# Kernel optimization log

Measured on AMD Instinct MI355X. Metric: run time of the kernel, lower is better.

Reference implementation:

```python
import jax, jax.numpy as jnp
import numpy as np

N_NODES = 100000
N_EDGES = 3200000
HID = 16
MP_ROUNDS = 3


def _mlp(w1, b1, w2, b2, x):
    # channels-first MLP applied per edge/node: x is [C_in, E]
    h = jax.nn.relu(w1 @ x + b1[:, None])
    return w2 @ h + b2[:, None]


def setup_inputs() -> dict:
    key = jax.random.key(0)
    ks = jax.random.split(key, 20)
    s = lambda k, shp: jax.random.normal(k, shp, dtype=jnp.float32) * 0.1
    inp = {
        "nodes": jax.random.normal(ks[0], (N_NODES,), dtype=jnp.float32),
        "edges_init": jax.random.normal(ks[1], (N_EDGES,), dtype=jnp.float32),
        "senders": jax.random.randint(ks[2], (N_EDGES,), 0, N_NODES, dtype=jnp.int32),
        "receivers": jax.random.randint(ks[3], (N_EDGES,), 0, N_NODES, dtype=jnp.int32),
        # EdgeEncoder: 1 -> HID -> HID
        "enc_w1": s(ks[4], (HID, 1)), "enc_b1": jnp.zeros((HID,), jnp.float32),
        "enc_w2": s(ks[5], (HID, HID)), "enc_b2": jnp.zeros((HID,), jnp.float32),
        # Node update MLP: (1 + 2*HID) -> HID -> 1  (shared across rounds)
        "node_w1": s(ks[6], (HID, 1 + 2 * HID)), "node_b1": jnp.zeros((HID,), jnp.float32),
        "node_w2": s(ks[7], (1, HID)), "node_b2": jnp.zeros((1,), jnp.float32),
        # Edge update MLP: (HID + 2) -> HID -> HID  (shared across rounds)
        "edge_w1": s(ks[8], (HID, HID + 2)), "edge_b1": jnp.zeros((HID,), jnp.float32),
        "edge_w2": s(ks[9], (HID, HID)), "edge_b2": jnp.zeros((HID,), jnp.float32),
        # EdgeDecoder: HID -> HID -> 1
        "dec_w1": s(ks[10], (HID, HID)), "dec_b1": jnp.zeros((HID,), jnp.float32),
        "dec_w2": s(ks[11], (1, HID)), "dec_b2": jnp.zeros((1,), jnp.float32),
        "alpha": jnp.float32(0.1),
    }
    return inp


def reference(nodes, edges_init, senders, receivers,
              enc_w1, enc_b1, enc_w2, enc_b2,
              node_w1, node_b1, node_w2, node_b2,
              edge_w1, edge_b1, edge_w2, edge_b2,
              dec_w1, dec_b1, dec_w2, dec_b2, alpha):
    n_nodes = nodes.shape[0]
    norm = jnp.abs(edges_init).max()
    e = edges_init / norm                      # [E]
    e = _mlp(enc_w1, enc_b1, enc_w2, enc_b2, e[None, :])   # [HID, E]
    for _ in range(MP_ROUNDS):                 # shared-weight MP blocks
        # gather/scatter: aggregate edge features to nodes
        agg_s = jax.ops.segment_sum(e.T, senders, num_segments=n_nodes).T     # [HID, N]
        agg_r = jax.ops.segment_sum(e.T, receivers, num_segments=n_nodes).T   # [HID, N]
        node_in = jnp.concatenate([nodes[None, :], agg_s, agg_r], axis=0)     # [1+2H, N]
        nodes = _mlp(node_w1, node_b1, node_w2, node_b2, node_in)[0]          # [N]
        edge_in = jnp.concatenate([e, nodes[senders][None, :], nodes[receivers][None, :]], axis=0)  # [H+2, E]
        e = _mlp(edge_w1, edge_b1, edge_w2, edge_b2, edge_in)                 # [HID, E]
    e = _mlp(dec_w1, dec_b1, dec_w2, dec_b2, e)[0]          # [E]
    low_tri_data = edges_init + alpha * (e * norm)          # L = L + alpha*GNN(L)
    return low_tri_data
```

## Files before the change

kernel.cpp:

```cpp
#include <hip/hip_runtime.h>
#include <hip/hip_bf16.h>

#define N_NODES 100000
#define N_EDGES 3200000
#define HID 16
#define NB 256
#define NPB 391
#define SCAP 15360
#define RCAP 15360
#define FDEPTH 32
#define LCAP1 8704
#define LCAP2 26624

static constexpr int BLK = 256;

__device__ __forceinline__ float frelu(float x) { return fmaxf(x, 0.f); }
__device__ __forceinline__ float bflo(unsigned int u) {
  return __uint_as_float(u << 16);
}
__device__ __forceinline__ float bfhi(unsigned int u) {
  return __uint_as_float(u & 0xFFFF0000u);
}

__device__ __forceinline__ int find_bucket(const int* __restrict__ bstart,
                                           int i) {
  int lo = 0, hi = NB;
#pragma unroll
  for (int s = 0; s < 8; ++s) {
    int mid = (lo + hi) >> 1;
    if (i >= bstart[mid]) lo = mid; else hi = mid;
  }
  return lo;
}

union E16 {
  float4 f4[2];
  __hip_bfloat16 h[16];
};

__global__ __launch_bounds__(256) void k_norm(const float* __restrict__ edges,
                                              unsigned int* __restrict__ normbits) {
  float m = 0.f;
  for (int i = blockIdx.x * blockDim.x + threadIdx.x; i < N_EDGES;
       i += gridDim.x * blockDim.x)
    m = fmaxf(m, fabsf(edges[i]));
#pragma unroll
  for (int off = 32; off > 0; off >>= 1)
    m = fmaxf(m, __shfl_down(m, off, 64));
  __shared__ float smax[BLK / 64];
  if ((threadIdx.x & 63) == 0) smax[threadIdx.x >> 6] = m;
  __syncthreads();
  if (threadIdx.x == 0) {
    float b = smax[0];
#pragma unroll
    for (int w = 1; w < BLK / 64; ++w) b = fmaxf(b, smax[w]);
    atomicMax(normbits, __float_as_uint(b));
  }
}

__global__ __launch_bounds__(1024) void k_split(
    const int* __restrict__ senders, const int* __restrict__ receivers,
    const float* __restrict__ edges, int* __restrict__ gcnt,
    unsigned int* __restrict__ pM, float* __restrict__ pV,
    unsigned int* __restrict__ pO) {
  __shared__ __align__(16) unsigned int fM[NB][FDEPTH];
  __shared__ __align__(16) unsigned int fV[NB][FDEPTH];
  __shared__ __align__(16) unsigned int fO[NB][FDEPTH];
  __shared__ int fcnt[NB];
  const int t = threadIdx.x;
  if (t < NB) fcnt[t] = 0;
  __syncthreads();
  const int e0 = blockIdx.x * (N_EDGES / 256);
  const int e1 = e0 + (N_EDGES / 256);
  for (int base = e0; base < e1; base += 1024) {
    const int i = base + t;
    if (i < e1) {
      int s = senders[i];
      unsigned int b = (unsigned int)s / NPB;
      unsigned int m = (((unsigned int)s - b * NPB) << 22) | (unsigned int)i;
      unsigned int v = __float_as_uint(edges[i]);
      unsigned int o = (unsigned int)receivers[i];
      int pos = atomicAdd(&fcnt[b], 1);
      if (pos < FDEPTH) {
        fM[b][pos] = m; fV[b][pos] = v; fO[b][pos] = o;
      } else {
        int gb = atomicAdd(&gcnt[b], 1);
        if (gb < SCAP) {
          pM[(size_t)b * SCAP + gb] = m;
          pV[(size_t)b * SCAP + gb] = __uint_as_float(v);
          pO[(size_t)b * SCAP + gb] = o;
        }
      }
    }
    __syncthreads();
    const bool last = (base + 1024 >= e1);
    if (t < NB) {
      int c = fcnt[t]; if (c > FDEPTH) c = FDEPTH;
      int nf = last ? c : (c & ~15);
      if (nf > 0) {
        int gb = atomicAdd(&gcnt[t], nf);
        size_t db = (size_t)t * SCAP + gb;
        if ((gb & 3) == 0 && gb + nf <= SCAP) {
          int k = 0;
          for (; k + 4 <= nf; k += 4) {
            *(uint4*)(pM + db + k) = *(const uint4*)(&fM[t][k]);
            *(uint4*)((unsigned int*)pV + db + k) = *(const uint4*)(&fV[t][k]);
            *(uint4*)(pO + db + k) = *(const uint4*)(&fO[t][k]);
          }
          for (; k < nf; ++k) {
            pM[db + k] = fM[t][k]; pV[db + k] = __uint_as_float(fV[t][k]);
            pO[db + k] = fO[t][k];
          }
        } else {
          for (int k = 0; k < nf; ++k)
            if (gb + k < SCAP) {
              pM[db + k] = fM[t][k]; pV[db + k] = __uint_as_float(fV[t][k]);
              pO[db + k] = fO[t][k];
            }
        }
        int res = c - nf;
        for (int k = 0; k < res; ++k) {
          fM[t][k] = fM[t][nf + k]; fV[t][k] = fV[t][nf + k];
          fO[t][k] = fO[t][nf + k];
        }
        fcnt[t] = res;
      } else fcnt[t] = c;
    }
    __syncthreads();
  }
}

__global__ __launch_bounds__(1024) void k_bsort1(
    const unsigned int* __restrict__ pM, const float* __restrict__ pV,
    const unsigned int* __restrict__ pO, const int* __restrict__ gcnt,
    unsigned int* __restrict__ srecv, unsigned int* __restrict__ sorig,
    unsigned short* __restrict__ svalbf, int* __restrict__ soff,
    int* __restrict__ bstart) {
  __shared__ unsigned int sM[LCAP1];
  __shared__ float sV[LCAP1];
  __shared__ unsigned int sO[LCAP1];
  __shared__ int hist[NPB], pref[NPB + 1], sc[NPB], cur[NPB];
  __shared__ int bb[NB];
  __shared__ int base_s;
  const int b = blockIdx.x, t = threadIdx.x, nt = blockDim.x;
  if (t < NB) { int c = gcnt[t]; bb[t] = c > SCAP ? SCAP : c; }
  for (int k = t; k < NPB; k += nt) hist[k] = 0;
  __syncthreads();
  if (t == 0) { int s = 0; for (int k = 0; k < b; ++k) s += bb[k]; base_s = s; }
  int nb = gcnt[b]; if (nb > SCAP) nb = SCAP;
  const unsigned int* PM = pM + (size_t)b * SCAP;
  const float* PV = pV + (size_t)b * SCAP;
  const unsigned int* PO = pO + (size_t)b * SCAP;
  for (int i = t; i < nb; i += nt) atomicAdd(&hist[PM[i] >> 22], 1);
  __syncthreads();
  if (t < NPB) sc[t] = hist[t];
  __syncthreads();
  for (int d = 1; d < NPB; d <<= 1) {
    int add = 0;
    if (t < NPB && t >= d) add = sc[t - d];
    __syncthreads();
    if (t < NPB && t >= d) sc[t] += add;
    __syncthreads();
  }
  if (t < NPB) pref[t] = sc[t] - hist[t];
  if (t == 0) pref[NPB] = sc[NPB - 1];
  __syncthreads();
  const int base = base_s;
  const int node0 = b * NPB;
  for (int k = t; k < NPB; k += nt) {
    int n = node0 + k;
    if (n < N_NODES) soff[n] = base + pref[k];
  }
  if (t == 0) bstart[b] = base;
  if (b == NB - 1 && t == 0) {
    soff[N_NODES] = base + nb;
    bstart[NB] = base + nb;
  }
  __syncthreads();
  int klo = 0;
  while (klo < NPB) {
    int base0 = pref[klo];
    int khi = klo;
    while (khi < NPB && pref[khi + 1] - base0 <= LCAP1) ++khi;
    if (khi == klo) khi = klo + 1;
    for (int k = klo + t; k < khi; k += nt) cur[k] = pref[k];
    __syncthreads();
    for (int i = t; i < nb; i += nt) {
      unsigned int m = PM[i];
      int key = (int)(m >> 22);
      if (key >= klo && key < khi) {
        int p = atomicAdd(&cur[key], 1) - base0;
        if (p < LCAP1) { sM[p] = m; sV[p] = PV[i]; sO[p] = PO[i]; }
      }
    }
    __syncthreads();
    int csz = pref[khi] - base0;
    for (int i = t; i < csz; i += nt) {
      int g = base + base0 + i;
      srecv[g] = sO[i]; sorig[g] = sM[i] & 0x3FFFFFu;
      __hip_bfloat16 hb = __float2bfloat16(sV[i]);
      svalbf[g] = *(unsigned short*)&hb;
    }
    __syncthreads();
    klo = khi;
  }
}

__global__ __launch_bounds__(256) void k_sfill(
    const int* __restrict__ soff, unsigned short* __restrict__ ssend16) {
  int wave = (blockIdx.x * blockDim.x + threadIdx.x) >> 6;
  int lane = threadIdx.x & 63, half = lane >> 5, l32 = lane & 31;
  int n = wave * 2 + half;
  unsigned short local = (unsigned short)(n - (n / NPB) * NPB);
  int s0 = soff[n], s1 = soff[n + 1];
  for (int k = s0 + l32; k < s1; k += 32) ssend16[k] = local;
}

__global__ __launch_bounds__(1024) void k_rsplit(
    const unsigned int* __restrict__ srecv, int* __restrict__ gcnt2,
    unsigned int* __restrict__ rpA) {
  __shared__ __align__(16) unsigned int fA[NB][FDEPTH];
  __shared__ int fcnt[NB];
  const int t = threadIdx.x;
  if (t < NB) fcnt[t] = 0;
  __syncthreads();
  const int e0 = blockIdx.x * (N_EDGES / 256);
  const int e1 = e0 + (N_EDGES / 256);
  for (int base = e0; base < e1; base += 1024) {
    const int i = base + t;
    if (i < e1) {
      unsigned int r = srecv[i];
      unsigned int b = r / NPB;
      unsigned int a = ((r - b * NPB) << 22) | (unsigned int)i;
      int pos = atomicAdd(&fcnt[b], 1);
      if (pos < FDEPTH) {
        fA[b][pos] = a;
      } else {
        int gb = atomicAdd(&gcnt2[b], 1);
        if (gb < RCAP) rpA[(size_t)b * RCAP + gb] = a;
      }
    }
    __syncthreads();
    const bool last = (base + 1024 >= e1);
    if (t < NB) {
      int c = fcnt[t]; if (c > FDEPTH) c = FDEPTH;
      int nf = last ? c : (c & ~15);
      if (nf > 0) {
        int gb = atomicAdd(&gcnt2[t], nf);
        size_t db = (size_t)t * RCAP + gb;
        if ((gb & 3) == 0 && gb + nf <= RCAP) {
          int k = 0;
          for (; k + 4 <= nf; k += 4)
            *(uint4*)(rpA + db + k) = *(const uint4*)(&fA[t][k]);
          for (; k < nf; ++k) rpA[db + k] = fA[t][k];
        } else {
          for (int k = 0; k < nf; ++k)
            if (gb + k < RCAP) rpA[db + k] = fA[t][k];
        }
        int res = c - nf;
        for (int k = 0; k < res; ++k) fA[t][k] = fA[t][nf + k];
        fcnt[t] = res;
      } else fcnt[t] = c;
    }
    __syncthreads();
  }
}

__global__ __launch_bounds__(1024) void k_rsort(
    const unsigned int* __restrict__ rpA, const int* __restrict__ gcnt2,
    unsigned int* __restrict__ rlist, int* __restrict__ roff) {
  __shared__ unsigned int sA[LCAP2];
  __shared__ int hist[NPB], pref[NPB + 1], sc[NPB], cur[NPB];
  __shared__ int bb[NB];
  __shared__ int base_s;
  const int b = blockIdx.x, t = threadIdx.x, nt = blockDim.x;
  if (t < NB) { int c = gcnt2[t]; bb[t] = c > RCAP ? RCAP : c; }
  for (int k = t; k < NPB; k += nt) hist[k] = 0;
  __syncthreads();
  if (t == 0) { int s = 0; for (int k = 0; k < b; ++k) s += bb[k]; base_s = s; }
  int nb = gcnt2[b]; if (nb > RCAP) nb = RCAP;
  const unsigned int* PA = rpA + (size_t)b * RCAP;
  for (int i = t; i < nb; i += nt) atomicAdd(&hist[PA[i] >> 22], 1);
  __syncthreads();
  if (t < NPB) sc[t] = hist[t];
  __syncthreads();
  for (int d = 1; d < NPB; d <<= 1) {
    int add = 0;
    if (t < NPB && t >= d) add = sc[t - d];
    __syncthreads();
    if (t < NPB && t >= d) sc[t] += add;
    __syncthreads();
  }
  if (t < NPB) pref[t] = sc[t] - hist[t];
  if (t == 0) pref[NPB] = sc[NPB - 1];
  __syncthreads();
  const int base = base_s;
  const int node0 = b * NPB;
  for (int k = t; k < NPB; k += nt) {
    int n = node0 + k;
    if (n < N_NODES) roff[n] = base + pref[k];
  }
  if (b == NB - 1 && t == 0) roff[N_NODES] = base + nb;
  __syncthreads();
  int klo = 0;
  while (klo < NPB) {
    int base0 = pref[klo];
    int khi = klo;
    while (khi < NPB && pref[khi + 1] - base0 <= LCAP2) ++khi;
    if (khi == klo) khi = klo + 1;
    for (int k = klo + t; k < khi; k += nt) cur[k] = pref[k];
    __syncthreads();
    for (int i = t; i < nb; i += nt) {
      unsigned int a = PA[i];
      int key = (int)(a >> 22);
      if (key >= klo && key < khi) {
        int p = atomicAdd(&cur[key], 1) - base0;
        if (p < LCAP2) sA[p] = a;
      }
    }
    __syncthreads();
    int csz = pref[khi] - base0;
    for (int i = t; i < csz; i += nt)
      rlist[base + base0 + i] = sA[i] & 0x3FFFFFu;
    __syncthreads();
    klo = khi;
  }
}

__global__ __launch_bounds__(256) void k_encode(
    const unsigned short* __restrict__ svalbf, const float* __restrict__ w1,
    const float* __restrict__ b1, const float* __restrict__ w2,
    const float* __restrict__ b2, const unsigned int* __restrict__ normbits,
    unsigned short* __restrict__ e) {
  int i = blockIdx.x * blockDim.x + threadIdx.x;
  float norm = __uint_as_float(*normbits);
  float x = bflo((unsigned int)svalbf[i]) / norm;
  float h[HID];
#pragma unroll
  for (int j = 0; j < HID; ++j) h[j] = frelu(fmaf(w1[j], x, b1[j]));
  E16 o;
#pragma unroll
  for (int j = 0; j < HID; ++j) {
    float acc = b2[j];
#pragma unroll
    for (int k = 0; k < HID; ++k) acc = fmaf(w2[j * HID + k], h[k], acc);
    o.h[j] = __float2bfloat16(acc);
  }
  float4* ep = (float4*)(e + (size_t)i * HID);
  ep[0] = o.f4[0];
  ep[1] = o.f4[1];
}

__global__ __launch_bounds__(256) void k_aggN(
    const unsigned short* __restrict__ e, const int* __restrict__ roff,
    const unsigned int* __restrict__ rlist, const int* __restrict__ soff,
    const float* __restrict__ nodesr, const float* __restrict__ nw1,
    const float* __restrict__ nb1_, const float* __restrict__ nw2,
    const float* __restrict__ nb2_, float* __restrict__ nodesw) {
  int wave = (blockIdx.x * blockDim.x + threadIdx.x) >> 6;
  int lane = threadIdx.x & 63, half = lane >> 5, l32 = lane & 31;
  int n = wave * 2 + half;
  int sub = l32 & 1, j16 = l32 >> 1;
  int r0 = roff[n], rdeg = roff[n + 1] - r0;
  float ar[8] = {0, 0, 0, 0, 0, 0, 0, 0};
  for (int q0 = 0; q0 < rdeg; q0 += 16) {
    int slot = q0 + j16;
    bool ok = slot < rdeg;
    int idx = r0 + (ok ? slot : 0);
    unsigned int si = rlist[idx];
    uint4 raw = *(const uint4*)(e + (size_t)si * HID + sub * 8);
    float v[8] = {bflo(raw.x), bfhi(raw.x), bflo(raw.y), bfhi(raw.y),
                  bflo(raw.z), bfhi(raw.z), bflo(raw.w), bfhi(raw.w)};
#pragma unroll
    for (int c = 0; c < 8; ++c) ar[c] += ok ? v[c] : 0.f;
  }
#pragma unroll
  for (int off = 16; off >= 2; off >>= 1)
#pragma unroll
    for (int c = 0; c < 8; ++c) ar[c] += __shfl_down(ar[c], off, 64);
  int s0 = soff[n], sdeg = soff[n + 1] - s0;
  float as[16];
#pragma unroll
  for (int c = 0; c < 16; ++c) as[c] = 0.f;
  for (int c0 = 0; c0 < sdeg; c0 += 32) {
    int k = c0 + l32;
    bool ok = k < sdeg;
    int idx = s0 + (ok ? k : 0);
    uint4 ra = *(const uint4*)(e + (size_t)idx * HID);
    uint4 rb = *(const uint4*)(e + (size_t)idx * HID + 8);
    float x[16] = {bflo(ra.x), bfhi(ra.x), bflo(ra.y), bfhi(ra.y),
                   bflo(ra.z), bfhi(ra.z), bflo(ra.w), bfhi(ra.w),
                   bflo(rb.x), bfhi(rb.x), bflo(rb.y), bfhi(rb.y),
                   bflo(rb.z), bfhi(rb.z), bflo(rb.w), bfhi(rb.w)};
#pragma unroll
    for (int c = 0; c < 16; ++c) as[c] += ok ? x[c] : 0.f;
  }
#pragma unroll
  for (int off = 16; off >= 1; off >>= 1)
#pragma unroll
    for (int c = 0; c < 16; ++c) as[c] += __shfl_down(as[c], off, 64);
  float aS[16], aR[16];
#pragma unroll
  for (int c = 0; c < 16; ++c) aS[c] = __shfl(as[c], half * 32, 64);
#pragma unroll
  for (int k = 0; k < 8; ++k) aR[k] = __shfl(ar[k], half * 32, 64);
#pragma unroll
  for (int k = 0; k < 8; ++k) aR[8 + k] = __shfl(ar[k], half * 32 + 1, 64);
  float nsv = nodesr[n];
  float pv = 0.f;
  if (l32 < 16) {
    int j = l32;
    float a1 = fmaf(nw1[j * 33], nsv, nb1_[j]);
#pragma unroll
    for (int k = 0; k < 16; ++k) a1 = fmaf(nw1[j * 33 + 1 + k], aS[k], a1);
#pragma unroll
    for (int k = 0; k < 16; ++k) a1 = fmaf(nw1[j * 33 + 17 + k], aR[k], a1);
    pv = nw2[j] * frelu(a1);
  }
#pragma unroll
  for (int off = 8; off >= 1; off >>= 1) pv += __shfl_down(pv, off, 64);
  if (l32 == 0) nodesw[n] = pv + nb2_[0];
}

__global__ __launch_bounds__(256, 2) void k_edgeE(
    unsigned short* __restrict__ e, const unsigned int* __restrict__ srecv,
    const unsigned short* __restrict__ ssend16, const int* __restrict__ bstart,
    const float* __restrict__ nodes, const float* __restrict__ w1,
    const float* __restrict__ b1, const float* __restrict__ w2,
    const float* __restrict__ b2) {
  int i = blockIdx.x * blockDim.x + threadIdx.x;
  int bk = find_bucket(bstart, i);
  int snd = bk * NPB + (int)ssend16[i];
  float ns = nodes[snd], nr = nodes[srecv[i]];
  uint4* ep = (uint4*)(e + (size_t)i * HID);
  uint4 ra = ep[0], rb = ep[1];
  unsigned int pk[8] = {ra.x, ra.y, ra.z, ra.w, rb.x, rb.y, rb.z, rb.w};
  float h[16];
#pragma unroll
  for (int j = 0; j < 16; ++j)
    h[j] = fmaf(w1[j * 18 + 16], ns, fmaf(w1[j * 18 + 17], nr, b1[j]));
#pragma unroll
  for (int kp = 0; kp < 8; ++kp) {
    float x0 = bflo(pk[kp]), x1 = bfhi(pk[kp]);
#pragma unroll
    for (int j = 0; j < 16; ++j)
      h[j] = fmaf(w1[j * 18 + 2 * kp + 1], x1,
                  fmaf(w1[j * 18 + 2 * kp], x0, h[j]));
  }
#pragma unroll
  for (int j = 0; j < 16; ++j) h[j] = frelu(h[j]);
  float y[16];
#pragma unroll
  for (int c = 0; c < 16; ++c) y[c] = b2[c];
#pragma unroll
  for (int j = 0; j < 16; ++j)
#pragma unroll
    for (int c = 0; c < 16; ++c) y[c] = fmaf(w2[c * HID + j], h[j], y[c]);
  E16 o;
#pragma unroll
  for (int c = 0; c < 16; ++c) o.h[c] = __float2bfloat16(y[c]);
  float4* fp = (float4*)ep;
  fp[0] = o.f4[0];
  fp[1] = o.f4[1];
}

__global__ __launch_bounds__(256, 2) void k_final(
    const unsigned short* __restrict__ e, const unsigned int* __restrict__ srecv,
    const unsigned short* __restrict__ ssend16, const int* __restrict__ bstart,
    const unsigned int* __restrict__ sorig, const float* __restrict__ nodes,
    const float* __restrict__ ew1, const float* __restrict__ eb1,
    const float* __restrict__ ew2, const float* __restrict__ eb2,
    const float* __restrict__ dw1, const float* __restrict__ db1,
    const float* __restrict__ dw2, const float* __restrict__ db2,
    const unsigned int* __restrict__ normbits, const float* __restrict__ alpha,
    float* __restrict__ out) {
  int i = blockIdx.x * blockDim.x + threadIdx.x;
  int bk = find_bucket(bstart, i);
  int snd = bk * NPB + (int)ssend16[i];
  float ns = nodes[snd], nr = nodes[srecv[i]];
  const uint4* ep = (const uint4*)(e + (size_t)i * HID);
  uint4 ra = ep[0], rb = ep[1];
  unsigned int pk[8] = {ra.x, ra.y, ra.z, ra.w, rb.x, rb.y, rb.z, rb.w};
  float h[16];
#pragma unroll
  for (int j = 0; j < 16; ++j)
    h[j] = fmaf(ew1[j * 18 + 16], ns, fmaf(ew1[j * 18 + 17], nr, eb1[j]));
#pragma unroll
  for (int kp = 0; kp < 8; ++kp) {
    float x0 = bflo(pk[kp]), x1 = bfhi(pk[kp]);
#pragma unroll
    for (int j = 0; j < 16; ++j)
      h[j] = fmaf(ew1[j * 18 + 2 * kp + 1], x1,
                  fmaf(ew1[j * 18 + 2 * kp], x0, h[j]));
  }
#pragma unroll
  for (int j = 0; j < 16; ++j) h[j] = frelu(h[j]);
  float y[16];
#pragma unroll
  for (int c = 0; c < 16; ++c) y[c] = eb2[c];
#pragma unroll
  for (int j = 0; j < 16; ++j)
#pragma unroll
    for (int c = 0; c < 16; ++c) y[c] = fmaf(ew2[c * HID + j], h[j], y[c]);
  float d = db2[0];
#pragma unroll
  for (int j = 0; j < 16; ++j) {
    float a1 = db1[j];
#pragma unroll
    for (int k = 0; k < 16; ++k) a1 = fmaf(dw1[j * HID + k], y[k], a1);
    d = fmaf(dw2[j], frelu(a1), d);
  }
  float alphaN = alpha[0] * __uint_as_float(*normbits);
  out[sorig[i]] = alphaN * d;
}

__global__ __launch_bounds__(256) void k_resid(const float* __restrict__ edges,
                                               float* __restrict__ out) {
  int i = blockIdx.x * blockDim.x + threadIdx.x;
  out[i] += edges[i];
}

extern "C" void kernel_launch(void* const* d_in, const int* in_sizes, int n_in,
                              void* d_out, int out_size, void* d_ws,
                              size_t ws_size, hipStream_t stream) {
  const float* nodes0 = (const float*)d_in[0];
  const float* edges0 = (const float*)d_in[1];
  const int* senders = (const int*)d_in[2];
  const int* receivers = (const int*)d_in[3];
  const float* enc_w1 = (const float*)d_in[4];
  const float* enc_b1 = (const float*)d_in[5];
  const float* enc_w2 = (const float*)d_in[6];
  const float* enc_b2 = (const float*)d_in[7];
  const float* node_w1 = (const float*)d_in[8];
  const float* node_b1 = (const float*)d_in[9];
  const float* node_w2 = (const float*)d_in[10];
  const float* node_b2 = (const float*)d_in[11];
  const float* edge_w1 = (const float*)d_in[12];
  const float* edge_b1 = (const float*)d_in[13];
  const float* edge_w2 = (const float*)d_in[14];
  const float* edge_b2 = (const float*)d_in[15];
  const float* dec_w1 = (const float*)d_in[16];
  const float* dec_b1 = (const float*)d_in[17];
  const float* dec_w2 = (const float*)d_in[18];
  const float* dec_b2 = (const float*)d_in[19];
  const float* alpha = (const float*)d_in[20];

  char* ws = (char*)d_ws;
  unsigned short* e = (unsigned short*)ws;
  char* p = ws + (size_t)N_EDGES * HID * 2;
  unsigned int* srecv = (unsigned int*)p;    p += (size_t)N_EDGES * 4;
  unsigned int* sorig = (unsigned int*)p;    p += (size_t)N_EDGES * 4;
  unsigned int* rlist = (unsigned int*)p;    p += (size_t)N_EDGES * 4;
  unsigned short* ssend16 = (unsigned short*)p; p += (size_t)N_EDGES * 2;
  unsigned short* svalbf = (unsigned short*)p;  p += (size_t)N_EDGES * 2;
  int* soff = (int*)p;                       p += (size_t)(N_NODES + 16) * 4;
  int* roff = (int*)p;                       p += (size_t)(N_NODES + 16) * 4;
  float* nbA = (float*)p;                    p += (size_t)N_NODES * 4;
  float* nbB = (float*)p;                    p += (size_t)N_NODES * 4;
  unsigned int* normbits = (unsigned int*)p; p += 64;
  int* gcnt = (int*)p;                       p += NB * 4;
  int* gcnt2 = (int*)p;                      p += NB * 4;
  int* bstart = (int*)p;                     p += (NB + 1) * 4;
  unsigned int* pM = (unsigned int*)ws;
  float* pV = (float*)(ws + (size_t)NB * SCAP * 4);
  unsigned int* pO = (unsigned int*)(ws + (size_t)NB * SCAP * 8);
  unsigned int* rpA = (unsigned int*)(ws + (size_t)NB * SCAP * 12);

  const int ngrid = 12500;
  const int egrid = N_EDGES / BLK;

  hipMemsetAsync(normbits, 0, 64 + 2 * NB * 4, stream);
  k_norm<<<512, BLK, 0, stream>>>(edges0, normbits);
  k_split<<<256, 1024, 0, stream>>>(senders, receivers, edges0, gcnt, pM, pV, pO);
  k_bsort1<<<NB, 1024, 0, stream>>>(pM, pV, pO, gcnt, srecv, sorig, svalbf,
                                    soff, bstart);
  k_sfill<<<ngrid, BLK, 0, stream>>>(soff, ssend16);
  k_rsplit<<<256, 1024, 0, stream>>>(srecv, gcnt2, rpA);
  k_rsort<<<NB, 1024, 0, stream>>>(rpA, gcnt2, rlist, roff);
  k_encode<<<egrid, BLK, 0, stream>>>(svalbf, enc_w1, enc_b1, enc_w2, enc_b2,
                                      normbits, e);
  k_aggN<<<ngrid, BLK, 0, stream>>>(e, roff, rlist, soff, nodes0, node_w1,
                                    node_b1, node_w2, node_b2, nbA);
  k_edgeE<<<egrid, BLK, 0, stream>>>(e, srecv, ssend16, bstart, nbA, edge_w1,
                                     edge_b1, edge_w2, edge_b2);
  k_aggN<<<ngrid, BLK, 0, stream>>>(e, roff, rlist, soff, nbA, node_w1,
                                    node_b1, node_w2, node_b2, nbB);
  k_edgeE<<<egrid, BLK, 0, stream>>>(e, srecv, ssend16, bstart, nbB, edge_w1,
                                     edge_b1, edge_w2, edge_b2);
  k_aggN<<<ngrid, BLK, 0, stream>>>(e, roff, rlist, soff, nbB, node_w1,
                                    node_b1, node_w2, node_b2, nbA);
  k_final<<<egrid, BLK, 0, stream>>>(e, srecv, ssend16, bstart, sorig, nbA,
                                     edge_w1, edge_b1, edge_w2, edge_b2,
                                     dec_w1, dec_b1, dec_w2, dec_b2, normbits,
                                     alpha, (float*)d_out);
  k_resid<<<egrid, BLK, 0, stream>>>(edges0, (float*)d_out);
}
```

Before: 918.2 us.

## Store full sender ids in bsort, drop sfill, multi-edge per thread edge kernels

The bucket sort now writes a 32-bit sender index per edge, which removes the k_sfill kernel and the per-edge binary search over bucket starts in the edge kernels. k_edgeE now processes 4 edges per thread and k_final 2, so weight loads are amortised across edges. k_aggN splits its gather loops into full unmasked iterations plus a masked tail. The trade-offs are extra bytes for the 32-bit sender array and higher register pressure in the multi-edge kernels.

```diff
diff --git a/kernel.cpp b/kernel.cpp
--- a/kernel.cpp
+++ b/kernel.cpp
@@ -21,16 +21,10 @@
 __device__ __forceinline__ float bfhi(unsigned int u) {
   return __uint_as_float(u & 0xFFFF0000u);
 }
-
-__device__ __forceinline__ int find_bucket(const int* __restrict__ bstart,
-                                           int i) {
-  int lo = 0, hi = NB;
-#pragma unroll
-  for (int s = 0; s < 8; ++s) {
-    int mid = (lo + hi) >> 1;
-    if (i >= bstart[mid]) lo = mid; else hi = mid;
-  }
-  return lo;
+__device__ __forceinline__ unsigned int packbf(float lo, float hi) {
+  __hip_bfloat16 hl = __float2bfloat16(lo), hh = __float2bfloat16(hi);
+  return ((unsigned int)(*(unsigned short*)&hh) << 16) |
+         (unsigned int)(*(unsigned short*)&hl);
 }
 
 union E16 {
@@ -134,8 +128,8 @@
     const unsigned int* __restrict__ pM, const float* __restrict__ pV,
     const unsigned int* __restrict__ pO, const int* __restrict__ gcnt,
     unsigned int* __restrict__ srecv, unsigned int* __restrict__ sorig,
-    unsigned short* __restrict__ svalbf, int* __restrict__ soff,
-    int* __restrict__ bstart) {
+    unsigned short* __restrict__ svalbf, unsigned int* __restrict__ ssend32,
+    int* __restrict__ soff) {
   __shared__ unsigned int sM[LCAP1];
   __shared__ float sV[LCAP1];
   __shared__ unsigned int sO[LCAP1];
@@ -171,11 +165,7 @@
     int n = node0 + k;
     if (n < N_NODES) soff[n] = base + pref[k];
   }
-  if (t == 0) bstart[b] = base;
-  if (b == NB - 1 && t == 0) {
-    soff[N_NODES] = base + nb;
-    bstart[NB] = base + nb;
-  }
+  if (b == NB - 1 && t == 0) soff[N_NODES] = base + nb;
   __syncthreads();
   int klo = 0;
   while (klo < NPB) {
@@ -197,23 +187,15 @@
     int csz = pref[khi] - base0;
     for (int i = t; i < csz; i += nt) {
       int g = base + base0 + i;
-      srecv[g] = sO[i]; sorig[g] = sM[i] & 0x3FFFFFu;
+      unsigned int m = sM[i];
+      srecv[g] = sO[i]; sorig[g] = m & 0x3FFFFFu;
+      ssend32[g] = (unsigned int)(node0 + (int)(m >> 22));
       __hip_bfloat16 hb = __float2bfloat16(sV[i]);
       svalbf[g] = *(unsigned short*)&hb;
     }
     __syncthreads();
     klo = khi;
   }
-}
-
-__global__ __launch_bounds__(256) void k_sfill(
-    const int* __restrict__ soff, unsigned short* __restrict__ ssend16) {
-  int wave = (blockIdx.x * blockDim.x + threadIdx.x) >> 6;
-  int lane = threadIdx.x & 63, half = lane >> 5, l32 = lane & 31;
-  int n = wave * 2 + half;
-  unsigned short local = (unsigned short)(n - (n / NPB) * NPB);
-  int s0 = soff[n], s1 = soff[n + 1];
-  for (int k = s0 + l32; k < s1; k += 32) ssend16[k] = local;
 }
 
 __global__ __launch_bounds__(1024) void k_rsplit(
@@ -363,16 +345,28 @@
   int sub = l32 & 1, j16 = l32 >> 1;
   int r0 = roff[n], rdeg = roff[n + 1] - r0;
   float ar[8] = {0, 0, 0, 0, 0, 0, 0, 0};
-  for (int q0 = 0; q0 < rdeg; q0 += 16) {
+  int fullA = rdeg & ~15;
+  int q0 = 0;
+  for (; q0 < fullA; q0 += 16) {
+    int idx = r0 + q0 + j16;
+    unsigned int si = rlist[idx];
+    uint4 raw = *(const uint4*)(e + (size_t)si * HID + sub * 8);
+    ar[0] += bflo(raw.x); ar[1] += bfhi(raw.x);
+    ar[2] += bflo(raw.y); ar[3] += bfhi(raw.y);
+    ar[4] += bflo(raw.z); ar[5] += bfhi(raw.z);
+    ar[6] += bflo(raw.w); ar[7] += bfhi(raw.w);
+  }
+  if (q0 < rdeg) {
     int slot = q0 + j16;
     bool ok = slot < rdeg;
     int idx = r0 + (ok ? slot : 0);
     unsigned int si = rlist[idx];
     uint4 raw = *(const uint4*)(e + (size_t)si * HID + sub * 8);
-    float v[8] = {bflo(raw.x), bfhi(raw.x), bflo(raw.y), bfhi(raw.y),
-                  bflo(raw.z), bfhi(raw.z), bflo(raw.w), bfhi(raw.w)};
-#pragma unroll
-    for (int c = 0; c < 8; ++c) ar[c] += ok ? v[c] : 0.f;
+    float okf = ok ? 1.f : 0.f;
+    ar[0] = fmaf(bflo(raw.x), okf, ar[0]); ar[1] = fmaf(bfhi(raw.x), okf, ar[1]);
+    ar[2] = fmaf(bflo(raw.y), okf, ar[2]); ar[3] = fmaf(bfhi(raw.y), okf, ar[3]);
+    ar[4] = fmaf(bflo(raw.z), okf, ar[4]); ar[5] = fmaf(bfhi(raw.z), okf, ar[5]);
+    ar[6] = fmaf(bflo(raw.w), okf, ar[6]); ar[7] = fmaf(bfhi(raw.w), okf, ar[7]);
   }
 #pragma unroll
   for (int off = 16; off >= 2; off >>= 1)
@@ -382,18 +376,36 @@
   float as[16];
 #pragma unroll
   for (int c = 0; c < 16; ++c) as[c] = 0.f;
-  for (int c0 = 0; c0 < sdeg; c0 += 32) {
+  int fullB = sdeg & ~31;
+  int c0 = 0;
+  for (; c0 < fullB; c0 += 32) {
+    int idx = s0 + c0 + l32;
+    uint4 ra = *(const uint4*)(e + (size_t)idx * HID);
+    uint4 rb = *(const uint4*)(e + (size_t)idx * HID + 8);
+    as[0] += bflo(ra.x);  as[1] += bfhi(ra.x);
+    as[2] += bflo(ra.y);  as[3] += bfhi(ra.y);
+    as[4] += bflo(ra.z);  as[5] += bfhi(ra.z);
+    as[6] += bflo(ra.w);  as[7] += bfhi(ra.w);
+    as[8] += bflo(rb.x);  as[9] += bfhi(rb.x);
+    as[10] += bflo(rb.y); as[11] += bfhi(rb.y);
+    as[12] += bflo(rb.z); as[13] += bfhi(rb.z);
+    as[14] += bflo(rb.w); as[15] += bfhi(rb.w);
+  }
+  if (c0 < sdeg) {
     int k = c0 + l32;
     bool ok = k < sdeg;
     int idx = s0 + (ok ? k : 0);
     uint4 ra = *(const uint4*)(e + (size_t)idx * HID);
     uint4 rb = *(const uint4*)(e + (size_t)idx * HID + 8);
-    float x[16] = {bflo(ra.x), bfhi(ra.x), bflo(ra.y), bfhi(ra.y),
-                   bflo(ra.z), bfhi(ra.z), bflo(ra.w), bfhi(ra.w),
-                   bflo(rb.x), bfhi(rb.x), bflo(rb.y), bfhi(rb.y),
-                   bflo(rb.z), bfhi(rb.z), bflo(rb.w), bfhi(rb.w)};
-#pragma unroll
-    for (int c = 0; c < 16; ++c) as[c] += ok ? x[c] : 0.f;
+    float okf = ok ? 1.f : 0.f;
+    as[0] = fmaf(bflo(ra.x), okf, as[0]);  as[1] = fmaf(bfhi(ra.x), okf, as[1]);
+    as[2] = fmaf(bflo(ra.y), okf, as[2]);  as[3] = fmaf(bfhi(ra.y), okf, as[3]);
+    as[4] = fmaf(bflo(ra.z), okf, as[4]);  as[5] = fmaf(bfhi(ra.z), okf, as[5]);
+    as[6] = fmaf(bflo(ra.w), okf, as[6]);  as[7] = fmaf(bfhi(ra.w), okf, as[7]);
+    as[8] = fmaf(bflo(rb.x), okf, as[8]);  as[9] = fmaf(bfhi(rb.x), okf, as[9]);
+    as[10] = fmaf(bflo(rb.y), okf, as[10]); as[11] = fmaf(bfhi(rb.y), okf, as[11]);
+    as[12] = fmaf(bflo(rb.z), okf, as[12]); as[13] = fmaf(bfhi(rb.z), okf, as[13]);
+    as[14] = fmaf(bflo(rb.w), okf, as[14]); as[15] = fmaf(bfhi(rb.w), okf, as[15]);
   }
 #pragma unroll
   for (int off = 16; off >= 1; off >>= 1)
@@ -424,94 +436,164 @@
 
 __global__ __launch_bounds__(256, 2) void k_edgeE(
     unsigned short* __restrict__ e, const unsigned int* __restrict__ srecv,
-    const unsigned short* __restrict__ ssend16, const int* __restrict__ bstart,
-    const float* __restrict__ nodes, const float* __restrict__ w1,
-    const float* __restrict__ b1, const float* __restrict__ w2,
-    const float* __restrict__ b2) {
-  int i = blockIdx.x * blockDim.x + threadIdx.x;
-  int bk = find_bucket(bstart, i);
-  int snd = bk * NPB + (int)ssend16[i];
-  float ns = nodes[snd], nr = nodes[srecv[i]];
-  uint4* ep = (uint4*)(e + (size_t)i * HID);
-  uint4 ra = ep[0], rb = ep[1];
-  unsigned int pk[8] = {ra.x, ra.y, ra.z, ra.w, rb.x, rb.y, rb.z, rb.w};
-  float h[16];
+    const unsigned int* __restrict__ ssend32, const float* __restrict__ nodes,
+    const float* __restrict__ w1, const float* __restrict__ b1,
+    const float* __restrict__ w2, const float* __restrict__ b2) {
+  int i0 = (blockIdx.x * blockDim.x + threadIdx.x) * 4;
+  float ns[4], nr[4];
+#pragma unroll
+  for (int q = 0; q < 4; ++q) {
+    ns[q] = nodes[ssend32[i0 + q]];
+    nr[q] = nodes[srecv[i0 + q]];
+  }
+  unsigned int pk[4][8];
+#pragma unroll
+  for (int q = 0; q < 4; ++q) {
+    const uint4* ep = (const uint4*)(e + (size_t)(i0 + q) * HID);
+    uint4 ra = ep[0], rb = ep[1];
+    pk[q][0] = ra.x; pk[q][1] = ra.y; pk[q][2] = ra.z; pk[q][3] = ra.w;
+    pk[q][4] = rb.x; pk[q][5] = rb.y; pk[q][6] = rb.z; pk[q][7] = rb.w;
+  }
+  float h[4][16];
+#pragma unroll
+  for (int j = 0; j < 16; ++j) {
+    float wA = w1[j * 18 + 16], wB = w1[j * 18 + 17], bb = b1[j];
+#pragma unroll
+    for (int q = 0; q < 4; ++q)
+      h[q][j] = fmaf(wA, ns[q], fmaf(wB, nr[q], bb));
+  }
+#pragma unroll
+  for (int kp = 0; kp < 8; ++kp) {
+    float x0[4], x1[4];
+#pragma unroll
+    for (int q = 0; q < 4; ++q) {
+      x0[q] = bflo(pk[q][kp]);
+      x1[q] = bfhi(pk[q][kp]);
+    }
+#pragma unroll
+    for (int j = 0; j < 16; ++j) {
+      float wA = w1[j * 18 + 2 * kp], wB = w1[j * 18 + 2 * kp + 1];
+#pragma unroll
+      for (int q = 0; q < 4; ++q)
+        h[q][j] = fmaf(wB, x1[q], fmaf(wA, x0[q], h[q][j]));
+    }
+  }
 #pragma unroll
   for (int j = 0; j < 16; ++j)
-    h[j] = fmaf(w1[j * 18 + 16], ns, fmaf(w1[j * 18 + 17], nr, b1[j]));
-#pragma unroll
-  for (int kp = 0; kp < 8; ++kp) {
-    float x0 = bflo(pk[kp]), x1 = bfhi(pk[kp]);
-#pragma unroll
-    for (int j = 0; j < 16; ++j)
-      h[j] = fmaf(w1[j * 18 + 2 * kp + 1], x1,
-                  fmaf(w1[j * 18 + 2 * kp], x0, h[j]));
-  }
-#pragma unroll
-  for (int j = 0; j < 16; ++j) h[j] = frelu(h[j]);
-  float y[16];
-#pragma unroll
-  for (int c = 0; c < 16; ++c) y[c] = b2[c];
-#pragma unroll
-  for (int j = 0; j < 16; ++j)
-#pragma unroll
-    for (int c = 0; c < 16; ++c) y[c] = fmaf(w2[c * HID + j], h[j], y[c]);
-  E16 o;
-#pragma unroll
-  for (int c = 0; c < 16; ++c) o.h[c] = __float2bfloat16(y[c]);
-  float4* fp = (float4*)ep;
-  fp[0] = o.f4[0];
-  fp[1] = o.f4[1];
+#pragma unroll
+    for (int q = 0; q < 4; ++q) h[q][j] = frelu(h[q][j]);
+#pragma unroll
+  for (int c0 = 0; c0 < 16; c0 += 8) {
+    float y[4][8];
+#pragma unroll
+    for (int cc = 0; cc < 8; ++cc) {
+      float bv = b2[c0 + cc];
+#pragma unroll
+      for (int q = 0; q < 4; ++q) y[q][cc] = bv;
+    }
+#pragma unroll
+    for (int j = 0; j < 16; ++j) {
+#pragma unroll
+      for (int cc = 0; cc < 8; ++cc) {
+        float wv = w2[(c0 + cc) * HID + j];
+#pragma unroll
+        for (int q = 0; q < 4; ++q) y[q][cc] = fmaf(wv, h[q][j], y[q][cc]);
+      }
+    }
+#pragma unroll
+    for (int q = 0; q < 4; ++q) {
+      uint4 o = make_uint4(packbf(y[q][0], y[q][1]), packbf(y[q][2], y[q][3]),
+                           packbf(y[q][4], y[q][5]), packbf(y[q][6], y[q][7]));
+      *(uint4*)(e + (size_t)(i0 + q) * HID + c0) = o;
+    }
+  }
 }
 
 __global__ __launch_bounds__(256, 2) void k_final(
     const unsigned short* __restrict__ e, const unsigned int* __restrict__ srecv,
-    const unsigned short* __restrict__ ssend16, const int* __restrict__ bstart,
-    const unsigned int* __restrict__ sorig, const float* __restrict__ nodes,
-    const float* __restrict__ ew1, const float* __restrict__ eb1,
-    const float* __restrict__ ew2, const float* __restrict__ eb2,
-    const float* __restrict__ dw1, const float* __restrict__ db1,
-    const float* __restrict__ dw2, const float* __restrict__ db2,
-    const unsigned int* __restrict__ normbits, const float* __restrict__ alpha,
-    float* __restrict__ out) {
-  int i = blockIdx.x * blockDim.x + threadIdx.x;
-  int bk = find_bucket(bstart, i);
-  int snd = bk * NPB + (int)ssend16[i];
-  float ns = nodes[snd], nr = nodes[srecv[i]];
-  const uint4* ep = (const uint4*)(e + (size_t)i * HID);
-  uint4 ra = ep[0], rb = ep[1];
-  unsigned int pk[8] = {ra.x, ra.y, ra.z, ra.w, rb.x, rb.y, rb.z, rb.w};
-  float h[16];
+    const unsigned int* __restrict__ ssend32, const unsigned int* __restrict__ sorig,
+    const float* __restrict__ nodes, const float* __restrict__ ew1,
+    const float* __restrict__ eb1, const float* __restrict__ ew2,
+    const float* __restrict__ eb2, const float* __restrict__ dw1,
+    const float* __restrict__ db1, const float* __restrict__ dw2,
+    const float* __restrict__ db2, const unsigned int* __restrict__ normbits,
+    const float* __restrict__ alpha, float* __restrict__ out) {
+  int i0 = (blockIdx.x * blockDim.x + threadIdx.x) * 2;
+  float ns[2], nr[2];
+#pragma unroll
+  for (int q = 0; q < 2; ++q) {
+    ns[q] = nodes[ssend32[i0 + q]];
+    nr[q] = nodes[srecv[i0 + q]];
+  }
+  unsigned int pk[2][8];
+#pragma unroll
+  for (int q = 0; q < 2; ++q) {
+    const uint4* ep = (const uint4*)(e + (size_t)(i0 + q) * HID);
+    uint4 ra = ep[0], rb = ep[1];
+    pk[q][0] = ra.x; pk[q][1] = ra.y; pk[q][2] = ra.z; pk[q][3] = ra.w;
+    pk[q][4] = rb.x; pk[q][5] = rb.y; pk[q][6] = rb.z; pk[q][7] = rb.w;
+  }
+  float h[2][16];
+#pragma unroll
+  for (int j = 0; j < 16; ++j) {
+    float wA = ew1[j * 18 + 16], wB = ew1[j * 18 + 17], bb = eb1[j];
+#pragma unroll
+    for (int q = 0; q < 2; ++q)
+      h[q][j] = fmaf(wA, ns[q], fmaf(wB, nr[q], bb));
+  }
+#pragma unroll
+  for (int kp = 0; kp < 8; ++kp) {
+    float x0[2], x1[2];
+#pragma unroll
+    for (int q = 0; q < 2; ++q) {
+      x0[q] = bflo(pk[q][kp]);
+      x1[q] = bfhi(pk[q][kp]);
+    }
+#pragma unroll
+    for (int j = 0; j < 16; ++j) {
+      float wA = ew1[j * 18 + 2 * kp], wB = ew1[j * 18 + 2 * kp + 1];
+#pragma unroll
+      for (int q = 0; q < 2; ++q)
+        h[q][j] = fmaf(wB, x1[q], fmaf(wA, x0[q], h[q][j]));
+    }
+  }
 #pragma unroll
   for (int j = 0; j < 16; ++j)
-    h[j] = fmaf(ew1[j * 18 + 16], ns, fmaf(ew1[j * 18 + 17], nr, eb1[j]));
-#pragma unroll
-  for (int kp = 0; kp < 8; ++kp) {
-    float x0 = bflo(pk[kp]), x1 = bfhi(pk[kp]);
-#pragma unroll
-    for (int j = 0; j < 16; ++j)
-      h[j] = fmaf(ew1[j * 18 + 2 * kp + 1], x1,
-                  fmaf(ew1[j * 18 + 2 * kp], x0, h[j]));
-  }
-#pragma unroll
-  for (int j = 0; j < 16; ++j) h[j] = frelu(h[j]);
-  float y[16];
-#pragma unroll
-  for (int c = 0; c < 16; ++c) y[c] = eb2[c];
-#pragma unroll
-  for (int j = 0; j < 16; ++j)
-#pragma unroll
-    for (int c = 0; c < 16; ++c) y[c] = fmaf(ew2[c * HID + j], h[j], y[c]);
-  float d = db2[0];
+#pragma unroll
+    for (int q = 0; q < 2; ++q) h[q][j] = frelu(h[q][j]);
+  float y[2][16];
+#pragma unroll
+  for (int c = 0; c < 16; ++c) {
+    float bv = eb2[c];
+#pragma unroll
+    for (int q = 0; q < 2; ++q) y[q][c] = bv;
+  }
 #pragma unroll
   for (int j = 0; j < 16; ++j) {
-    float a1 = db1[j];
-#pragma unroll
-    for (int k = 0; k < 16; ++k) a1 = fmaf(dw1[j * HID + k], y[k], a1);
-    d = fmaf(dw2[j], frelu(a1), d);
+#pragma unroll
+    for (int c = 0; c < 16; ++c) {
+      float wv = ew2[c * HID + j];
+#pragma unroll
+      for (int q = 0; q < 2; ++q) y[q][c] = fmaf(wv, h[q][j], y[q][c]);
+    }
+  }
+  float d[2] = {db2[0], db2[0]};
+#pragma unroll
+  for (int j = 0; j < 16; ++j) {
+    float a1[2] = {db1[j], db1[j]};
+#pragma unroll
+    for (int k = 0; k < 16; ++k) {
+      float wv = dw1[j * HID + k];
+#pragma unroll
+      for (int q = 0; q < 2; ++q) a1[q] = fmaf(wv, y[q][k], a1[q]);
+    }
+    float wd = dw2[j];
+#pragma unroll
+    for (int q = 0; q < 2; ++q) d[q] = fmaf(wd, frelu(a1[q]), d[q]);
   }
   float alphaN = alpha[0] * __uint_as_float(*normbits);
-  out[sorig[i]] = alphaN * d;
+#pragma unroll
+  for (int q = 0; q < 2; ++q) out[sorig[i0 + q]] = alphaN * d[q];
 }
 
 __global__ __launch_bounds__(256) void k_resid(const float* __restrict__ edges,
@@ -551,8 +633,8 @@
   unsigned int* srecv = (unsigned int*)p;    p += (size_t)N_EDGES * 4;
   unsigned int* sorig = (unsigned int*)p;    p += (size_t)N_EDGES * 4;
   unsigned int* rlist = (unsigned int*)p;    p += (size_t)N_EDGES * 4;
-  unsigned short* ssend16 = (unsigned short*)p; p += (size_t)N_EDGES * 2;
-  unsigned short* svalbf = (unsigned short*)p;  p += (size_t)N_EDGES * 2;
+  unsigned int* ssend32 = (unsigned int*)p;  p += (size_t)N_EDGES * 4;
+  unsigned short* svalbf = (unsigned short*)p; p += (size_t)N_EDGES * 2;
   int* soff = (int*)p;                       p += (size_t)(N_NODES + 16) * 4;
   int* roff = (int*)p;                       p += (size_t)(N_NODES + 16) * 4;
   float* nbA = (float*)p;                    p += (size_t)N_NODES * 4;
@@ -560,7 +642,6 @@
   unsigned int* normbits = (unsigned int*)p; p += 64;
   int* gcnt = (int*)p;                       p += NB * 4;
   int* gcnt2 = (int*)p;                      p += NB * 4;
-  int* bstart = (int*)p;                     p += (NB + 1) * 4;
   unsigned int* pM = (unsigned int*)ws;
   float* pV = (float*)(ws + (size_t)NB * SCAP * 4);
   unsigned int* pO = (unsigned int*)(ws + (size_t)NB * SCAP * 8);
@@ -568,30 +649,31 @@
 
   const int ngrid = 12500;
   const int egrid = N_EDGES / BLK;
+  const int egrid4 = N_EDGES / (BLK * 4);
+  const int egrid2 = N_EDGES / (BLK * 2);
 
   hipMemsetAsync(normbits, 0, 64 + 2 * NB * 4, stream);
   k_norm<<<512, BLK, 0, stream>>>(edges0, normbits);
   k_split<<<256, 1024, 0, stream>>>(senders, receivers, edges0, gcnt, pM, pV, pO);
   k_bsort1<<<NB, 1024, 0, stream>>>(pM, pV, pO, gcnt, srecv, sorig, svalbf,
-                                    soff, bstart);
-  k_sfill<<<ngrid, BLK, 0, stream>>>(soff, ssend16);
+                                    ssend32, soff);
   k_rsplit<<<256, 1024, 0, stream>>>(srecv, gcnt2, rpA);
   k_rsort<<<NB, 1024, 0, stream>>>(rpA, gcnt2, rlist, roff);
   k_encode<<<egrid, BLK, 0, stream>>>(svalbf, enc_w1, enc_b1, enc_w2, enc_b2,
                                       normbits, e);
   k_aggN<<<ngrid, BLK, 0, stream>>>(e, roff, rlist, soff, nodes0, node_w1,
                                     node_b1, node_w2, node_b2, nbA);
-  k_edgeE<<<egrid, BLK, 0, stream>>>(e, srecv, ssend16, bstart, nbA, edge_w1,
-                                     edge_b1, edge_w2, edge_b2);
+  k_edgeE<<<egrid4, BLK, 0, stream>>>(e, srecv, ssend32, nbA, edge_w1,
+                                      edge_b1, edge_w2, edge_b2);
   k_aggN<<<ngrid, BLK, 0, stream>>>(e, roff, rlist, soff, nbA, node_w1,
                                     node_b1, node_w2, node_b2, nbB);
-  k_edgeE<<<egrid, BLK, 0, stream>>>(e, srecv, ssend16, bstart, nbB, edge_w1,
-                                     edge_b1, edge_w2, edge_b2);
+  k_edgeE<<<egrid4, BLK, 0, stream>>>(e, srecv, ssend32, nbB, edge_w1,
+                                      edge_b1, edge_w2, edge_b2);
   k_aggN<<<ngrid, BLK, 0, stream>>>(e, roff, rlist, soff, nbB, node_w1,
                                     node_b1, node_w2, node_b2, nbA);
-  k_final<<<egrid, BLK, 0, stream>>>(e, srecv, ssend16, bstart, sorig, nbA,
-                                     edge_w1, edge_b1, edge_w2, edge_b2,
-                                     dec_w1, dec_b1, dec_w2, dec_b2, normbits,
-                                     alpha, (float*)d_out);
+  k_final<<<egrid2, BLK, 0, stream>>>(e, srecv, ssend32, sorig, nbA, edge_w1,
+                                      edge_b1, edge_w2, edge_b2, dec_w1,
+                                      dec_b1, dec_w2, dec_b2, normbits, alpha,
+                                      (float*)d_out);
   k_resid<<<egrid, BLK, 0, stream>>>(edges0, (float*)d_out);
 }
```

Measured after the change: 902.1 us. Within noise of the previous version (-1.8%).
